# Performance work log

Measured on AMD Instinct MI355X. Metric: run time of the kernel, lower is better.

The kernel has to match this reference:

```python
import jax, jax.numpy as jnp
import numpy as np

B, N_LAT, N_PAT = 32, 64, 4096
DIM_LAT = DIM_PAT = DIM_ATTN = 192
H = 6
HD = DIM_ATTN // H  # 32
SCALE = HD ** -0.5


def setup_inputs() -> dict:
    key = jax.random.key(0)
    ks = jax.random.split(key, 8)
    s = lambda fan_in: 1.0 / np.sqrt(fan_in)
    return {
        "x_latents": jax.random.normal(ks[0], (B, N_LAT, DIM_LAT), jnp.float32),
        "x_patches": jax.random.normal(ks[1], (B, N_PAT, DIM_PAT), jnp.float32),
        # weights stored [in, out] (torch Linear applies x @ W.T; math identical)
        "W_rv_lat": jax.random.uniform(ks[2], (DIM_LAT, 2 * DIM_ATTN), jnp.float32, -s(DIM_LAT), s(DIM_LAT)),
        "W_rv_pat": jax.random.uniform(ks[3], (DIM_PAT, 2 * DIM_ATTN), jnp.float32, -s(DIM_PAT), s(DIM_PAT)),
        "W_proj_lat": jax.random.uniform(ks[4], (DIM_ATTN, DIM_LAT), jnp.float32, -s(DIM_ATTN), s(DIM_ATTN)),
        "b_proj_lat": jax.random.uniform(ks[5], (DIM_LAT,), jnp.float32, -s(DIM_ATTN), s(DIM_ATTN)),
        "W_proj_pat": jax.random.uniform(ks[6], (DIM_ATTN, DIM_PAT), jnp.float32, -s(DIM_ATTN), s(DIM_ATTN)),
        "b_proj_pat": jax.random.uniform(ks[7], (DIM_PAT,), jnp.float32, -s(DIM_ATTN), s(DIM_ATTN)),
    }


def _split_rv(x, W, n):
    # x: [B, n, d_in] -> r, v each [B, H, n, HD]
    rv = (x @ W).reshape(x.shape[0], n, 2, H, HD)
    rv = jnp.transpose(rv, (2, 0, 3, 1, 4))  # [2, B, H, n, HD]
    return rv[0], rv[1]


def reference(x_latents, x_patches, W_rv_lat, W_rv_pat,
              W_proj_lat, b_proj_lat, W_proj_pat, b_proj_pat):
    r_lat, v_lat = _split_rv(x_latents, W_rv_lat, N_LAT)   # [B,H,N_lat,HD]
    r_pat, v_pat = _split_rv(x_patches, W_rv_pat, N_PAT)   # [B,H,N_pat,HD]

    # single score matrix, softmaxed along both axes (dropout = 0, eval mode)
    scores = jnp.einsum('bhld,bhpd->bhlp', r_lat, r_pat) * SCALE  # [B,H,N_lat,N_pat]
    attn = jax.nn.softmax(scores, axis=-1)    # row-wise (over patches)
    attn_T = jax.nn.softmax(scores, axis=-2)  # col-wise (over latents)

    out_lat = jnp.einsum('bhlp,bhpd->blhd', attn, v_pat).reshape(B, N_LAT, DIM_ATTN)
    out_pat = jnp.einsum('bhlp,bhld->bphd', attn_T, v_lat).reshape(B, N_PAT, DIM_ATTN)

    out_lat = out_lat @ W_proj_lat + b_proj_lat
    out_pat = out_pat @ W_proj_pat + b_proj_pat
    return out_lat, out_pat
```

## Files before the change

kernel.cpp:

```cpp
#include <hip/hip_runtime.h>

#define B_   32
#define NL_  64
#define NP_  4096
#define DIM_ 192
#define H_   6
#define HD_  32
#define PC_  128
#define NCH_ (NP_/PC_)
#define CPB_ 4
#define NSC_ (NCH_/CPB_)

typedef unsigned short u16;
typedef __attribute__((ext_vector_type(8))) short bf16x8;
typedef __attribute__((ext_vector_type(4))) short bf16x4;
typedef __attribute__((ext_vector_type(4))) float f32x4;

#define MFMA16(a,b,c) __builtin_amdgcn_mfma_f32_16x16x32_bf16(a,b,c,0,0,0)

__device__ __forceinline__ float bf2f(u16 s){ return __builtin_bit_cast(float,(unsigned)s<<16); }
__device__ __forceinline__ u16 f2bf(float f){
  unsigned u = __builtin_bit_cast(unsigned,f);
  return (u16)((u + 0x7FFFu + ((u>>16)&1u))>>16);
}

__global__ void k0_transpose(const float* __restrict__ W0, const float* __restrict__ W1,
                             const float* __restrict__ W2, const float* __restrict__ W3,
                             u16* __restrict__ T0, u16* __restrict__ T1,
                             u16* __restrict__ T2, u16* __restrict__ T3){
  int m = blockIdx.x >> 4, sub = blockIdx.x & 15;
  const float* src; u16* dst; int R, C;
  if      (m==0){src=W0;dst=T0;R=192;C=384;}
  else if (m==1){src=W1;dst=T1;R=192;C=384;}
  else if (m==2){src=W2;dst=T2;R=192;C=192;}
  else          {src=W3;dst=T3;R=192;C=192;}
  int total = R*C;
  for (int o = sub*256 + threadIdx.x; o < total; o += 16*256){
    int c = o / R, r = o - c*R;
    dst[o] = f2bf(src[r*C + c]);
  }
}

__global__ __launch_bounds__(512) void k_rv(const float* __restrict__ X,
    const u16* __restrict__ Wt, u16* __restrict__ R, u16* __restrict__ V,
    int Nseq, int nshift){
  __shared__ u16 As[128*200];
  __shared__ u16 Bs[64*200];
  const int t = threadIdx.x;
  const int m0 = blockIdx.x*128;
  const int lane = t & 63, w = t >> 6, g = lane >> 4, ln = lane & 15;
  const int srow = t >> 2, sc = (t & 3) * 8;
  const int srB = t >> 3, bq = t & 7;
  const f32x4 ZF = {0.f,0.f,0.f,0.f};

  #pragma unroll
  for (int k0 = 0; k0 < 192; k0 += 32){
    float4 x0 = *(const float4*)&X[(size_t)(m0 + srow)*192 + k0 + sc];
    float4 x1 = *(const float4*)&X[(size_t)(m0 + srow)*192 + k0 + sc + 4];
    bf16x8 av;
    av[0]=(short)f2bf(x0.x); av[1]=(short)f2bf(x0.y); av[2]=(short)f2bf(x0.z); av[3]=(short)f2bf(x0.w);
    av[4]=(short)f2bf(x1.x); av[5]=(short)f2bf(x1.y); av[6]=(short)f2bf(x1.z); av[7]=(short)f2bf(x1.w);
    *(bf16x8*)&As[srow*200 + k0 + sc] = av;
  }

  bf16x8 breg[3];
  #pragma unroll
  for (int it=0; it<3; it++)
    breg[it] = *(const bf16x8*)&Wt[(size_t)srB*192 + bq*24 + it*8];

  __syncthreads();

  for (int n0 = 0; n0 < 384; n0 += 64){
    #pragma unroll
    for (int it=0; it<3; it++)
      *(bf16x8*)&Bs[srB*200 + bq*24 + it*8] = breg[it];
    if (n0 < 320){
      #pragma unroll
      for (int it=0; it<3; it++)
        breg[it] = *(const bf16x8*)&Wt[(size_t)(n0 + 64 + srB)*192 + bq*24 + it*8];
    }
    __syncthreads();

    f32x4 acc[4];
    #pragma unroll
    for(int j=0;j<4;j++) acc[j]=ZF;
    #pragma unroll
    for (int k0 = 0; k0 < 192; k0 += 32){
      bf16x8 a0 = *(const bf16x8*)&As[(w*16 + ln)*200 + k0 + g*8];
      #pragma unroll
      for(int j=0;j<4;j++){
        bf16x8 bv = *(const bf16x8*)&Bs[(j*16 + ln)*200 + k0 + g*8];
        acc[j] = MFMA16(a0,bv,acc[j]);
      }
    }
    __syncthreads();

    #pragma unroll
    for(int j=0;j<4;j++){
      int n = n0 + j*16 + ln;
      u16* dst; int c;
      if (n < 192){ dst = R; c = n; } else { dst = V; c = n - 192; }
      int h = c >> 5, d = c & 31;
      #pragma unroll
      for(int r=0;r<4;r++){
        int m = m0 + w*16 + g*4 + r;
        int b = m >> nshift, sidx = m & (Nseq-1);
        dst[((((size_t)b*H_ + h)*(size_t)Nseq + sidx) << 5) + d] = f2bf(acc[j][r]);
      }
    }
  }
}

__global__ __launch_bounds__(256) void k_attn(
    const u16* __restrict__ r_lat_g, const u16* __restrict__ v_lat_g,
    const u16* __restrict__ r_pat_g, const u16* __restrict__ v_pat_g,
    u16* __restrict__ Opat,
    float* __restrict__ numT_ws,
    float* __restrict__ rowsum_ws){
  const float SCALE = 0.17677669529663687f;
  const int sc = blockIdx.x, h = blockIdx.y, b = blockIdx.z;
  const int bh = b*H_ + h;
  const int t = threadIdx.x, lane = t&63, w = t>>6, g = lane>>4, ln = lane&15;
  __shared__ u16 RL [64*40];
  __shared__ u16 VLT[32*72];
  __shared__ u16 EN [128*72];
  __shared__ u16 ET [64*136];
  __shared__ float RS[4*64];
  __shared__ u16 POOL[128*40];
  u16* RP  = POOL;
  u16* VPT = POOL;
  const f32x4 ZF = {0.f,0.f,0.f,0.f};

  const size_t latbase = (size_t)bh * (NL_*HD_);
  { int row = t>>2, col = (t&3)*8;
    *(bf16x8*)&RL[row*40+col] = *(const bf16x8*)&r_lat_g[latbase + row*32 + col]; }
  { int l = t>>2, dd = (t&3)*8;
    bf16x8 v = *(const bf16x8*)&v_lat_g[latbase + l*32 + dd];
    #pragma unroll
    for(int jj=0;jj<8;jj++) VLT[(dd+jj)*72 + l] = (u16)v[jj]; }

  const int p0 = t>>2, dd0 = (t&3)*8;
  const size_t pb0 = ((size_t)bh*NP_ + (size_t)sc*(CPB_*PC_))*HD_;
  bf16x8 rcur0 = *(const bf16x8*)&r_pat_g[pb0 + (size_t)p0*32 + dd0];
  bf16x8 rcur1 = *(const bf16x8*)&r_pat_g[pb0 + (size_t)(64+p0)*32 + dd0];
  bf16x8 vcur0 = *(const bf16x8*)&v_pat_g[pb0 + (size_t)p0*32 + dd0];
  bf16x8 vcur1 = *(const bf16x8*)&v_pat_g[pb0 + (size_t)(64+p0)*32 + dd0];

  f32x4 nm[2]; nm[0]=ZF; nm[1]=ZF;
  float rs[4] = {0.f,0.f,0.f,0.f};

  for (int c = 0; c < CPB_; ++c){
    *(bf16x8*)&RP[p0*40 + dd0]      = rcur0;
    *(bf16x8*)&RP[(64+p0)*40 + dd0] = rcur1;
    __syncthreads();

    f32x4 sf[2][4];
    { bf16x8 a0 = *(const bf16x8*)&RP[(w*32      + ln)*40 + g*8];
      bf16x8 a1 = *(const bf16x8*)&RP[(w*32 + 16 + ln)*40 + g*8];
      #pragma unroll
      for(int j=0;j<4;j++){
        bf16x8 bl = *(const bf16x8*)&RL[(j*16 + ln)*40 + g*8];
        sf[0][j] = MFMA16(a0, bl, ZF);
        sf[1][j] = MFMA16(a1, bl, ZF);
      } }

    bf16x8 rnxt0, rnxt1, vnxt0, vnxt1;
    const bool more = (c+1 < CPB_);
    if (more){
      const size_t pbn = pb0 + (size_t)(c+1)*(PC_*HD_);
      rnxt0 = *(const bf16x8*)&r_pat_g[pbn + (size_t)p0*32 + dd0];
      rnxt1 = *(const bf16x8*)&r_pat_g[pbn + (size_t)(64+p0)*32 + dd0];
      vnxt0 = *(const bf16x8*)&v_pat_g[pbn + (size_t)p0*32 + dd0];
      vnxt1 = *(const bf16x8*)&v_pat_g[pbn + (size_t)(64+p0)*32 + dd0];
    }

    float e[2][4][4], rcs[2][4];
    #pragma unroll
    for(int i=0;i<2;i++)
      #pragma unroll
      for(int r=0;r<4;r++){
        float cs = 0.f;
        #pragma unroll
        for(int j=0;j<4;j++){
          float ev = __expf(sf[i][j][r] * SCALE);
          e[i][j][r] = ev; cs += ev; rs[j] += ev;
        }
        cs += __shfl_xor(cs,1); cs += __shfl_xor(cs,2);
        cs += __shfl_xor(cs,4); cs += __shfl_xor(cs,8);
        rcs[i][r] = 1.0f / cs;
      }
    #pragma unroll
    for(int i=0;i<2;i++)
      #pragma unroll
      for(int j=0;j<4;j++){
        #pragma unroll
        for(int r=0;r<4;r++)
          EN[(w*32 + i*16 + g*4 + r)*72 + j*16 + ln] = f2bf(e[i][j][r]*rcs[i][r]);
        bf16x4 pk;
        #pragma unroll
        for(int r=0;r<4;r++) pk[r] = (short)f2bf(e[i][j][r]);
        *(bf16x4*)&ET[(j*16+ln)*136 + w*32 + i*16 + g*4] = pk;
      }
    __syncthreads();

    #pragma unroll
    for(int jj=0;jj<8;jj++){
      VPT[(dd0+jj)*136 + p0]      = (u16)vcur0[jj];
      VPT[(dd0+jj)*136 + 64 + p0] = (u16)vcur1[jj];
    }

    f32x4 op[2][2];
    #pragma unroll
    for(int i=0;i<2;i++){ op[i][0]=ZF; op[i][1]=ZF; }
    #pragma unroll
    for(int ks=0; ks<2; ks++){
      bf16x8 bv[2];
      #pragma unroll
      for(int jd=0;jd<2;jd++) bv[jd] = *(const bf16x8*)&VLT[(jd*16+ln)*72 + ks*32 + g*8];
      #pragma unroll
      for(int i=0;i<2;i++){
        bf16x8 af = *(const bf16x8*)&EN[(w*32 + i*16 + ln)*72 + ks*32 + g*8];
        #pragma unroll
        for(int jd=0;jd<2;jd++) op[i][jd] = MFMA16(af, bv[jd], op[i][jd]);
      }
    }
    const size_t obase = ((size_t)b*NP_ + (size_t)(sc*CPB_ + c)*PC_)*DIM_ + h*32;
    #pragma unroll
    for(int i=0;i<2;i++)
      #pragma unroll
      for(int jd=0;jd<2;jd++)
        #pragma unroll
        for(int r=0;r<4;r++){
          int p = w*32 + i*16 + g*4 + r, dd = jd*16 + ln;
          Opat[obase + (size_t)p*DIM_ + dd] = f2bf(op[i][jd][r]);
        }
    __syncthreads();

    #pragma unroll
    for(int ks=0; ks<4; ks++){
      bf16x8 af = *(const bf16x8*)&ET[(w*16+ln)*136 + ks*32 + g*8];
      #pragma unroll
      for(int dj=0;dj<2;dj++){
        bf16x8 bv = *(const bf16x8*)&VPT[(dj*16+ln)*136 + ks*32 + g*8];
        nm[dj] = MFMA16(af, bv, nm[dj]);
      }
    }
    __syncthreads();

    if (more){ rcur0=rnxt0; rcur1=rnxt1; vcur0=vnxt0; vcur1=vnxt1; }
  }

  #pragma unroll
  for(int j=0;j<4;j++){
    float vs = rs[j];
    vs += __shfl_xor(vs,16); vs += __shfl_xor(vs,32);
    if (g == 0) RS[w*64 + j*16 + ln] = vs;
  }
  __syncthreads();
  if (t < 64)
    rowsum_ws[((size_t)bh*NSC_ + sc)*64 + t] = RS[t] + RS[64+t] + RS[128+t] + RS[192+t];
  float* dstN = numT_ws + ((size_t)bh*NSC_ + sc)*2048;
  #pragma unroll
  for(int dj=0;dj<2;dj++)
    #pragma unroll
    for(int r=0;r<4;r++){
      int l = w*16 + g*4 + r, dd = dj*16 + ln;
      dstN[l*32 + dd] = nm[dj][r];
    }
}

__global__ __launch_bounds__(256) void k_lat_reduce(const float* __restrict__ numT_ws,
    const float* __restrict__ rowsum_ws, u16* __restrict__ attn_lat){
  int bh = blockIdx.x, b = bh / H_, h = bh - b*H_;
  __shared__ float RSs[64];
  int t = threadIdx.x;
  if (t < 64){
    float s = 0.f;
    for(int c=0;c<NSC_;c++) s += rowsum_ws[((size_t)bh*NSC_ + c)*64 + t];
    RSs[t] = 1.0f / s;
  }
  __syncthreads();
  for(int idx = t; idx < 2048; idx += 256){
    int l = idx >> 5, dd = idx & 31;
    float s = 0.f;
    for(int c=0;c<NSC_;c++) s += numT_ws[((size_t)bh*NSC_ + c)*2048 + idx];
    attn_lat[((size_t)b*NL_ + l)*DIM_ + h*32 + dd] = f2bf(s * RSs[l]);
  }
}

__global__ __launch_bounds__(256) void k_proj_lat(const u16* __restrict__ A,
    const u16* __restrict__ Wt, const float* __restrict__ bias, float* __restrict__ out){
  int b = blockIdx.x;
  __shared__ u16 As[64*40];
  __shared__ u16 Bs[192*40];
  int t = threadIdx.x, lane = t&63, w = t>>6, g = lane>>4, ln = lane&15;
  const f32x4 ZF = {0.f,0.f,0.f,0.f};
  f32x4 acc[4][3];
  #pragma unroll
  for(int i=0;i<4;i++)
    #pragma unroll
    for(int j=0;j<3;j++) acc[i][j]=ZF;
  for(int k0=0;k0<192;k0+=32){
    bf16x8 av; bf16x8 bv[3];
    { int row = t>>2, col=(t&3)*8;
      av = *(const bf16x8*)&A[((size_t)b*NL_ + row)*DIM_ + k0 + col]; }
    #pragma unroll
    for(int it=0;it<3;it++){
      int e = it*2048 + t*8, row = e>>5, col = (t&3)*8;
      bv[it] = *(const bf16x8*)&Wt[(size_t)row*192 + k0 + col];
    }
    if (k0) __syncthreads();
    { int row = t>>2, col=(t&3)*8; *(bf16x8*)&As[row*40+col] = av; }
    #pragma unroll
    for(int it=0;it<3;it++){
      int e = it*2048 + t*8, row = e>>5, col = (t&3)*8;
      *(bf16x8*)&Bs[row*40+col] = bv[it];
    }
    __syncthreads();
    bf16x8 bw[3];
    #pragma unroll
    for(int jf=0;jf<3;jf++) bw[jf] = *(const bf16x8*)&Bs[(w*48 + jf*16 + ln)*40 + g*8];
    #pragma unroll
    for(int lf=0;lf<4;lf++){
      bf16x8 af = *(const bf16x8*)&As[(lf*16 + ln)*40 + g*8];
      #pragma unroll
      for(int jf=0;jf<3;jf++) acc[lf][jf] = MFMA16(af, bw[jf], acc[lf][jf]);
    }
  }
  #pragma unroll
  for(int lf=0;lf<4;lf++)
    #pragma unroll
    for(int jf=0;jf<3;jf++){
      int j = w*48 + jf*16 + ln;
      float bs = bias[j];
      #pragma unroll
      for(int r=0;r<4;r++){
        int l = lf*16 + g*4 + r;
        out[((size_t)b*NL_ + l)*DIM_ + j] = acc[lf][jf][r] + bs;
      }
    }
}

__global__ __launch_bounds__(512) void k_proj_pat(const u16* __restrict__ X,
    const u16* __restrict__ Wt, const float* __restrict__ bias, float* __restrict__ out){
  __shared__ u16 As[128*200];
  __shared__ u16 Bs[64*200];
  const int t = threadIdx.x;
  const int m0 = blockIdx.x*128;
  const int lane = t & 63, w = t >> 6, g = lane >> 4, ln = lane & 15;
  const int srow = t >> 2, sc = (t & 3) * 8;
  const int srB = t >> 3, bq = t & 7;
  const f32x4 ZF = {0.f,0.f,0.f,0.f};

  #pragma unroll
  for (int k0 = 0; k0 < 192; k0 += 32)
    *(bf16x8*)&As[srow*200 + k0 + sc] = *(const bf16x8*)&X[(size_t)(m0 + srow)*192 + k0 + sc];

  bf16x8 breg[3];
  #pragma unroll
  for (int it=0; it<3; it++)
    breg[it] = *(const bf16x8*)&Wt[(size_t)srB*192 + bq*24 + it*8];

  __syncthreads();

  for (int n0 = 0; n0 < 192; n0 += 64){
    #pragma unroll
    for (int it=0; it<3; it++)
      *(bf16x8*)&Bs[srB*200 + bq*24 + it*8] = breg[it];
    if (n0 < 128){
      #pragma unroll
      for (int it=0; it<3; it++)
        breg[it] = *(const bf16x8*)&Wt[(size_t)(n0 + 64 + srB)*192 + bq*24 + it*8];
    }
    __syncthreads();

    f32x4 acc[4];
    #pragma unroll
    for(int j=0;j<4;j++) acc[j]=ZF;
    #pragma unroll
    for (int k0 = 0; k0 < 192; k0 += 32){
      bf16x8 a0 = *(const bf16x8*)&As[(w*16 + ln)*200 + k0 + g*8];
      #pragma unroll
      for(int j=0;j<4;j++){
        bf16x8 bv = *(const bf16x8*)&Bs[(j*16 + ln)*200 + k0 + g*8];
        acc[j] = MFMA16(a0,bv,acc[j]);
      }
    }
    __syncthreads();

    #pragma unroll
    for(int j=0;j<4;j++){
      int n = n0 + j*16 + ln;
      float bs = bias[n];
      #pragma unroll
      for(int r=0;r<4;r++){
        int m = m0 + w*16 + g*4 + r;
        out[(size_t)m*192 + n] = acc[j][r] + bs;
      }
    }
  }
}

extern "C" void kernel_launch(void* const* d_in, const int* in_sizes, int n_in,
                              void* d_out, int out_size, void* d_ws, size_t ws_size,
                              hipStream_t stream){
  const float* x_lat  = (const float*)d_in[0];
  const float* x_pat  = (const float*)d_in[1];
  const float* W_rv_l = (const float*)d_in[2];
  const float* W_rv_p = (const float*)d_in[3];
  const float* W_pj_l = (const float*)d_in[4];
  const float* b_pj_l = (const float*)d_in[5];
  const float* W_pj_p = (const float*)d_in[6];
  const float* b_pj_p = (const float*)d_in[7];
  float* out = (float*)d_out;

  char* ws = (char*)d_ws;
  size_t off = 0;
  auto alloc = [&](size_t bytes)->void*{ void* p = ws + off; off += (bytes + 255) & ~(size_t)255; return p; };
  u16* WtRL   = (u16*)alloc((size_t)384*192*2);
  u16* WtRP   = (u16*)alloc((size_t)384*192*2);
  u16* WtPL   = (u16*)alloc((size_t)192*192*2);
  u16* WtPP   = (u16*)alloc((size_t)192*192*2);
  u16* r_lat  = (u16*)alloc((size_t)B_*H_*NL_*HD_*2);
  u16* v_lat  = (u16*)alloc((size_t)B_*H_*NL_*HD_*2);
  u16* r_pat  = (u16*)alloc((size_t)B_*H_*NP_*HD_*2);
  u16* v_pat  = (u16*)alloc((size_t)B_*H_*NP_*HD_*2);
  u16* Opat   = (u16*)alloc((size_t)B_*NP_*DIM_*2);
  float* numT = (float*)alloc((size_t)B_*H_*NSC_*64*32*4);
  float* rsum = (float*)alloc((size_t)B_*H_*NSC_*64*4);
  u16* attn_l = (u16*)alloc((size_t)B_*NL_*DIM_*2);

  k0_transpose<<<64,256,0,stream>>>(W_rv_l, W_rv_p, W_pj_l, W_pj_p, WtRL, WtRP, WtPL, WtPP);
  k_rv<<<dim3((B_*NP_)/128),512,0,stream>>>(x_pat, WtRP, r_pat, v_pat, NP_, 12);
  k_rv<<<dim3((B_*NL_)/128),512,0,stream>>>(x_lat, WtRL, r_lat, v_lat, NL_, 6);
  k_attn<<<dim3(NSC_, H_, B_),256,0,stream>>>(r_lat, v_lat, r_pat, v_pat, Opat, numT, rsum);
  k_lat_reduce<<<B_*H_,256,0,stream>>>(numT, rsum, attn_l);
  k_proj_lat<<<B_,256,0,stream>>>(attn_l, WtPL, b_pj_l, out);
  k_proj_pat<<<dim3((B_*NP_)/128),512,0,stream>>>(Opat, WtPP, b_pj_p, out + (size_t)B_*NL_*DIM_);
}
```

Baseline: 184.6 us.

## Hold A tiles in registers, double the M tile, double-buffer B in GEMMs

Both the rv projection and the patch output projection now load each wave's A rows straight from global memory into registers as MFMA fragments, dropping the shared-memory A tile. Each block covers 256 rows instead of 128 (two 16-row fragments per wave), so every B fragment read from LDS feeds two MFMAs. The B weight tile is double-buffered, which removes one barrier per column chunk. This cuts LDS traffic and grid size, at the cost of more registers per thread (launch bounds now request 4 blocks) and fewer blocks; the A global reads are also less coalesced.

```diff
diff --git a/kernel.cpp b/kernel.cpp
--- a/kernel.cpp
+++ b/kernel.cpp
@@ -41,73 +41,84 @@
   }
 }
 
-__global__ __launch_bounds__(512) void k_rv(const float* __restrict__ X,
+__global__ __launch_bounds__(512,4) void k_rv(const float* __restrict__ X,
     const u16* __restrict__ Wt, u16* __restrict__ R, u16* __restrict__ V,
     int Nseq, int nshift){
-  __shared__ u16 As[128*200];
-  __shared__ u16 Bs[64*200];
+  __shared__ u16 Bs[2][64*200];
   const int t = threadIdx.x;
-  const int m0 = blockIdx.x*128;
+  const int m0 = blockIdx.x*256;
   const int lane = t & 63, w = t >> 6, g = lane >> 4, ln = lane & 15;
-  const int srow = t >> 2, sc = (t & 3) * 8;
   const int srB = t >> 3, bq = t & 7;
   const f32x4 ZF = {0.f,0.f,0.f,0.f};
 
-  #pragma unroll
-  for (int k0 = 0; k0 < 192; k0 += 32){
-    float4 x0 = *(const float4*)&X[(size_t)(m0 + srow)*192 + k0 + sc];
-    float4 x1 = *(const float4*)&X[(size_t)(m0 + srow)*192 + k0 + sc + 4];
-    bf16x8 av;
-    av[0]=(short)f2bf(x0.x); av[1]=(short)f2bf(x0.y); av[2]=(short)f2bf(x0.z); av[3]=(short)f2bf(x0.w);
-    av[4]=(short)f2bf(x1.x); av[5]=(short)f2bf(x1.y); av[6]=(short)f2bf(x1.z); av[7]=(short)f2bf(x1.w);
-    *(bf16x8*)&As[srow*200 + k0 + sc] = av;
-  }
+  bf16x8 af[2][6];
+  #pragma unroll
+  for (int i=0;i<2;i++)
+    #pragma unroll
+    for (int kk=0;kk<6;kk++){
+      const float* s = &X[(size_t)(m0 + w*32 + i*16 + ln)*192 + kk*32 + g*8];
+      float4 x0 = *(const float4*)s;
+      float4 x1 = *(const float4*)(s+4);
+      bf16x8 v;
+      v[0]=(short)f2bf(x0.x); v[1]=(short)f2bf(x0.y); v[2]=(short)f2bf(x0.z); v[3]=(short)f2bf(x0.w);
+      v[4]=(short)f2bf(x1.x); v[5]=(short)f2bf(x1.y); v[6]=(short)f2bf(x1.z); v[7]=(short)f2bf(x1.w);
+      af[i][kk] = v;
+    }
 
   bf16x8 breg[3];
   #pragma unroll
   for (int it=0; it<3; it++)
     breg[it] = *(const bf16x8*)&Wt[(size_t)srB*192 + bq*24 + it*8];
-
+  #pragma unroll
+  for (int it=0; it<3; it++)
+    *(bf16x8*)&Bs[0][srB*200 + bq*24 + it*8] = breg[it];
+  #pragma unroll
+  for (int it=0; it<3; it++)
+    breg[it] = *(const bf16x8*)&Wt[(size_t)(64 + srB)*192 + bq*24 + it*8];
   __syncthreads();
 
-  for (int n0 = 0; n0 < 384; n0 += 64){
-    #pragma unroll
-    for (int it=0; it<3; it++)
-      *(bf16x8*)&Bs[srB*200 + bq*24 + it*8] = breg[it];
-    if (n0 < 320){
+  for (int c = 0; c < 6; ++c){
+    if (c < 5){
+      u16* bn = &Bs[(c+1)&1][0];
       #pragma unroll
       for (int it=0; it<3; it++)
-        breg[it] = *(const bf16x8*)&Wt[(size_t)(n0 + 64 + srB)*192 + bq*24 + it*8];
-    }
-    __syncthreads();
-
-    f32x4 acc[4];
-    #pragma unroll
-    for(int j=0;j<4;j++) acc[j]=ZF;
-    #pragma unroll
-    for (int k0 = 0; k0 < 192; k0 += 32){
-      bf16x8 a0 = *(const bf16x8*)&As[(w*16 + ln)*200 + k0 + g*8];
+        *(bf16x8*)&bn[srB*200 + bq*24 + it*8] = breg[it];
+      if (c < 4){
+        #pragma unroll
+        for (int it=0; it<3; it++)
+          breg[it] = *(const bf16x8*)&Wt[(size_t)((c+2)*64 + srB)*192 + bq*24 + it*8];
+      }
+    }
+    const u16* bc = &Bs[c&1][0];
+    f32x4 acc[2][4];
+    #pragma unroll
+    for(int i=0;i<2;i++)
+      #pragma unroll
+      for(int j=0;j<4;j++) acc[i][j]=ZF;
+    #pragma unroll
+    for (int kk=0; kk<6; kk++)
+      #pragma unroll
+      for (int j=0; j<4; j++){
+        bf16x8 bv = *(const bf16x8*)&bc[(j*16 + ln)*200 + kk*32 + g*8];
+        acc[0][j] = MFMA16(af[0][kk], bv, acc[0][j]);
+        acc[1][j] = MFMA16(af[1][kk], bv, acc[1][j]);
+      }
+    #pragma unroll
+    for(int i=0;i<2;i++)
       #pragma unroll
       for(int j=0;j<4;j++){
-        bf16x8 bv = *(const bf16x8*)&Bs[(j*16 + ln)*200 + k0 + g*8];
-        acc[j] = MFMA16(a0,bv,acc[j]);
-      }
-    }
-    __syncthreads();
-
-    #pragma unroll
-    for(int j=0;j<4;j++){
-      int n = n0 + j*16 + ln;
-      u16* dst; int c;
-      if (n < 192){ dst = R; c = n; } else { dst = V; c = n - 192; }
-      int h = c >> 5, d = c & 31;
-      #pragma unroll
-      for(int r=0;r<4;r++){
-        int m = m0 + w*16 + g*4 + r;
-        int b = m >> nshift, sidx = m & (Nseq-1);
-        dst[((((size_t)b*H_ + h)*(size_t)Nseq + sidx) << 5) + d] = f2bf(acc[j][r]);
-      }
-    }
+        int n = c*64 + j*16 + ln;
+        u16* dst; int cc;
+        if (n < 192){ dst = R; cc = n; } else { dst = V; cc = n - 192; }
+        int h = cc >> 5, d = cc & 31;
+        #pragma unroll
+        for(int r=0;r<4;r++){
+          int m = m0 + w*32 + i*16 + g*4 + r;
+          int b = m >> nshift, sidx = m & (Nseq-1);
+          dst[((((size_t)b*H_ + h)*(size_t)Nseq + sidx) << 5) + d] = f2bf(acc[i][j][r]);
+        }
+      }
+    __syncthreads();
   }
 }
 
@@ -341,63 +352,73 @@
     }
 }
 
-__global__ __launch_bounds__(512) void k_proj_pat(const u16* __restrict__ X,
+__global__ __launch_bounds__(512,4) void k_proj_pat(const u16* __restrict__ X,
     const u16* __restrict__ Wt, const float* __restrict__ bias, float* __restrict__ out){
-  __shared__ u16 As[128*200];
-  __shared__ u16 Bs[64*200];
+  __shared__ u16 Bs[2][64*200];
   const int t = threadIdx.x;
-  const int m0 = blockIdx.x*128;
+  const int m0 = blockIdx.x*256;
   const int lane = t & 63, w = t >> 6, g = lane >> 4, ln = lane & 15;
-  const int srow = t >> 2, sc = (t & 3) * 8;
   const int srB = t >> 3, bq = t & 7;
   const f32x4 ZF = {0.f,0.f,0.f,0.f};
 
-  #pragma unroll
-  for (int k0 = 0; k0 < 192; k0 += 32)
-    *(bf16x8*)&As[srow*200 + k0 + sc] = *(const bf16x8*)&X[(size_t)(m0 + srow)*192 + k0 + sc];
+  bf16x8 af[2][6];
+  #pragma unroll
+  for (int i=0;i<2;i++)
+    #pragma unroll
+    for (int kk=0;kk<6;kk++)
+      af[i][kk] = *(const bf16x8*)&X[(size_t)(m0 + w*32 + i*16 + ln)*192 + kk*32 + g*8];
 
   bf16x8 breg[3];
   #pragma unroll
   for (int it=0; it<3; it++)
     breg[it] = *(const bf16x8*)&Wt[(size_t)srB*192 + bq*24 + it*8];
-
+  #pragma unroll
+  for (int it=0; it<3; it++)
+    *(bf16x8*)&Bs[0][srB*200 + bq*24 + it*8] = breg[it];
+  #pragma unroll
+  for (int it=0; it<3; it++)
+    breg[it] = *(const bf16x8*)&Wt[(size_t)(64 + srB)*192 + bq*24 + it*8];
   __syncthreads();
 
-  for (int n0 = 0; n0 < 192; n0 += 64){
-    #pragma unroll
-    for (int it=0; it<3; it++)
-      *(bf16x8*)&Bs[srB*200 + bq*24 + it*8] = breg[it];
-    if (n0 < 128){
+  for (int c = 0; c < 3; ++c){
+    if (c < 2){
+      u16* bn = &Bs[(c+1)&1][0];
       #pragma unroll
       for (int it=0; it<3; it++)
-        breg[it] = *(const bf16x8*)&Wt[(size_t)(n0 + 64 + srB)*192 + bq*24 + it*8];
-    }
-    __syncthreads();
-
-    f32x4 acc[4];
-    #pragma unroll
-    for(int j=0;j<4;j++) acc[j]=ZF;
-    #pragma unroll
-    for (int k0 = 0; k0 < 192; k0 += 32){
-      bf16x8 a0 = *(const bf16x8*)&As[(w*16 + ln)*200 + k0 + g*8];
+        *(bf16x8*)&bn[srB*200 + bq*24 + it*8] = breg[it];
+      if (c < 1){
+        #pragma unroll
+        for (int it=0; it<3; it++)
+          breg[it] = *(const bf16x8*)&Wt[(size_t)((c+2)*64 + srB)*192 + bq*24 + it*8];
+      }
+    }
+    const u16* bc = &Bs[c&1][0];
+    f32x4 acc[2][4];
+    #pragma unroll
+    for(int i=0;i<2;i++)
+      #pragma unroll
+      for(int j=0;j<4;j++) acc[i][j]=ZF;
+    #pragma unroll
+    for (int kk=0; kk<6; kk++)
+      #pragma unroll
+      for (int j=0; j<4; j++){
+        bf16x8 bv = *(const bf16x8*)&bc[(j*16 + ln)*200 + kk*32 + g*8];
+        acc[0][j] = MFMA16(af[0][kk], bv, acc[0][j]);
+        acc[1][j] = MFMA16(af[1][kk], bv, acc[1][j]);
+      }
+    #pragma unroll
+    for(int i=0;i<2;i++)
       #pragma unroll
       for(int j=0;j<4;j++){
-        bf16x8 bv = *(const bf16x8*)&Bs[(j*16 + ln)*200 + k0 + g*8];
-        acc[j] = MFMA16(a0,bv,acc[j]);
-      }
-    }
-    __syncthreads();
-
-    #pragma unroll
-    for(int j=0;j<4;j++){
-      int n = n0 + j*16 + ln;
-      float bs = bias[n];
-      #pragma unroll
-      for(int r=0;r<4;r++){
-        int m = m0 + w*16 + g*4 + r;
-        out[(size_t)m*192 + n] = acc[j][r] + bs;
-      }
-    }
+        int n = c*64 + j*16 + ln;
+        float bs = bias[n];
+        #pragma unroll
+        for(int r=0;r<4;r++){
+          int m = m0 + w*32 + i*16 + g*4 + r;
+          out[(size_t)m*192 + n] = acc[i][j][r] + bs;
+        }
+      }
+    __syncthreads();
   }
 }
 
@@ -431,10 +452,10 @@
   u16* attn_l = (u16*)alloc((size_t)B_*NL_*DIM_*2);
 
   k0_transpose<<<64,256,0,stream>>>(W_rv_l, W_rv_p, W_pj_l, W_pj_p, WtRL, WtRP, WtPL, WtPP);
-  k_rv<<<dim3((B_*NP_)/128),512,0,stream>>>(x_pat, WtRP, r_pat, v_pat, NP_, 12);
-  k_rv<<<dim3((B_*NL_)/128),512,0,stream>>>(x_lat, WtRL, r_lat, v_lat, NL_, 6);
+  k_rv<<<dim3((B_*NP_)/256),512,0,stream>>>(x_pat, WtRP, r_pat, v_pat, NP_, 12);
+  k_rv<<<dim3((B_*NL_)/256),512,0,stream>>>(x_lat, WtRL, r_lat, v_lat, NL_, 6);
   k_attn<<<dim3(NSC_, H_, B_),256,0,stream>>>(r_lat, v_lat, r_pat, v_pat, Opat, numT, rsum);
   k_lat_reduce<<<B_*H_,256,0,stream>>>(numT, rsum, attn_l);
   k_proj_lat<<<B_,256,0,stream>>>(attn_l, WtPL, b_pj_l, out);
-  k_proj_pat<<<dim3((B_*NP_)/128),512,0,stream>>>(Opat, WtPP, b_pj_p, out + (size_t)B_*NL_*DIM_);
-}
+  k_proj_pat<<<dim3((B_*NP_)/256),512,0,stream>>>(Opat, WtPP, b_pj_p, out + (size_t)B_*NL_*DIM_);
+}
```

After: 214.1 us. 1.16x slower.
